# Kernel tuning notes

Measured on AMD Instinct MI355X. Metric: run time of the kernel, lower is better.

## Reference

```python
import jax, jax.numpy as jnp
import numpy as np

# Module hyperparameters (from init_kwargs)
KH = KW = 3
STRIDE = 2
PAD = 1
OUT_PAD = 1
DIL = 1
IN_LEN = 8   # length of each input capsule
OUT_LEN = 8  # length of each output capsule
N_IN_CAPS = 64 // IN_LEN    # 8
N_OUT_CAPS = 64 // OUT_LEN  # 8
NUM_ITERATIONS = 3


def _squash(x):
    # v * |v|^2 / ((1 + |v|^2) * |v|), along last (capsule-length) dim
    sn = jnp.sum(x * x, axis=-1, keepdims=True)
    return x * (sn / ((1.0 + sn) * jnp.sqrt(sn + 1e-12)))


def _k_means_routing(priors, num_iterations):
    # priors: [..., K, M] ; soft k-means routing with 'dot' similarity,
    # softmax over the votes dim K (softmax_dim=-2), squash at the end.
    out = jnp.mean(priors, axis=-2, keepdims=True)          # [..., 1, M]
    for _ in range(num_iterations):
        nrm = jnp.linalg.norm(out, axis=-1, keepdims=True)
        out_n = out / jnp.maximum(nrm, 1e-12)               # F.normalize(p=2)
        logits = jnp.sum(priors * out_n, axis=-1, keepdims=True)  # [..., K, 1]
        probs = jax.nn.softmax(logits, axis=-2)
        out = jnp.sum(probs * priors, axis=-2, keepdims=True)
    return _squash(out)[..., 0, :]                          # [..., M]


def setup_inputs() -> dict:
    key = jax.random.key(0)
    k1, k2, k3 = jax.random.split(key, 3)
    input = jax.random.normal(k1, (2, 64, 32, 32), dtype=jnp.float32)
    # weight: (in_length, out_channels//out_length, out_length, kh, kw)
    weight = jax.random.normal(k2, (IN_LEN, N_OUT_CAPS, OUT_LEN, KH, KW), dtype=jnp.float32) * 0.1
    # bias: (out_channels//out_length, out_length)
    bias = jax.random.normal(k3, (N_OUT_CAPS, OUT_LEN), dtype=jnp.float32) * 0.1
    return {"input": input, "weight": weight, "bias": bias}


def reference(input, weight, bias):
    n, c_in, h_in, w_in = input.shape
    fi = c_in // IN_LEN
    fo = weight.shape[1]
    # conv_transpose == conv(lhs-dilated input, spatially flipped kernel)
    pad_lo = DIL * (KH - 1) - PAD
    patches = jax.lax.conv_general_dilated_patches(
        input, (KH, KW), (1, 1),
        padding=((pad_lo, pad_lo + OUT_PAD), (pad_lo, pad_lo + OUT_PAD)),
        lhs_dilation=(STRIDE, STRIDE), rhs_dilation=(DIL, DIL))
    ho, wo = patches.shape[-2], patches.shape[-1]
    # feature dim of patches is ordered (c, kh, kw), channel-major
    patches = patches.reshape(n, fi, IN_LEN, KH, KW, ho, wo)
    w_flip = weight[..., ::-1, ::-1]  # [IN_LEN, fo, OUT_LEN, KH, KW]
    # votes: each (input capsule, kernel tap) casts a vote per output capsule
    priors = jnp.einsum('nflhwpq,lgmhw->npqgfhwm', patches, w_flip)
    priors = priors.reshape(n, ho, wo, fo, fi * KH * KW, OUT_LEN)
    out = _k_means_routing(priors, NUM_ITERATIONS)  # [n, ho, wo, fo, OUT_LEN]
    out = out + bias                                # bias: [fo, OUT_LEN]
    out = out.reshape(n, ho, wo, fo * OUT_LEN).transpose(0, 3, 1, 2)
    return out  # [n, out_channels, ho, wo] = [2, 64, 64, 64]
```

## Files before the change

### kernel.cpp

```cpp
#include <hip/hip_runtime.h>
#include <math.h>

#define HIN 32
#define WIN 32
#define NITER 3

#define IROW 96

typedef float f2 __attribute__((ext_vector_type(2)));
static __device__ __forceinline__ f2 mk2(float a, float b) { f2 r; r.x = a; r.y = b; return r; }
static __device__ __forceinline__ f2 fma2(f2 a, f2 b, f2 c) { return __builtin_elementwise_fma(a, b, c); }

template <int CTRL>
__device__ __forceinline__ float dpp_add(float v) {
    int p = __builtin_amdgcn_update_dpp(0, __float_as_int(v), CTRL, 0xF, 0xF, true);
    return v + __int_as_float(p);
}
__device__ __forceinline__ float sum8(float v) {
    v = dpp_add<0xB1>(v);
    v = dpp_add<0x4E>(v);
    v = dpp_add<0x141>(v);
    return v;
}

template <int TH, int TW>
__device__ __forceinline__ void stage_weights(const float* __restrict__ weight,
                                              float* __restrict__ wlds, int t) {
    constexpr int T = TH * TW;
    const int sg = (t >> 3) & 7;
    const int sm = t & 7;
    const int l0 = t >> 6;
    const int dbase = sg * 80 + (((sm >> 1) + (sg >> 1)) & 3) * 20 + (sm & 1);
#pragma unroll
    for (int k = 0; k < 2 * T; ++k) {
        const int vtap = k >> 1;
        const int chunk = k & 1;
        const int hh = (TH == 1) ? 1 : ((vtap / TW) * 2);
        const int ww = (TW == 1) ? 1 : ((vtap % TW) * 2);
        const int jflip = (2 - hh) * 3 + (2 - ww);
        const int l = chunk * 4 + l0;
        wlds[vtap * 640 + dbase + l * 2] = weight[(chunk * 256 + t) * 9 + jflip];
    }
}

template <int NROWS, int NCHUNK>
__device__ __forceinline__ void stage_input(const float* __restrict__ in,
                                            float* __restrict__ ilds,
                                            int t, int n, int y0, int x0) {
    const int c = t >> 2, r = t & 3;
    const int cpad = c + 4 * (c >> 3);
#pragma unroll
    for (int pp = r; pp < NROWS * NCHUNK; pp += 4) {
        const int yi = pp / NCHUNK, ch = pp % NCHUNK;
        const int y = y0 + yi;
        const int xc = x0 + ch * 4;
        float4 vv = {0.f, 0.f, 0.f, 0.f};
        if (y < HIN && xc < WIN)
            vv = *(const float4*)(in + (((size_t)(n * 64 + c) * HIN + y) * WIN + xc));
        ilds[(yi * 12 + ch * 4 + 0) * IROW + cpad] = vv.x;
        ilds[(yi * 12 + ch * 4 + 1) * IROW + cpad] = vv.y;
        ilds[(yi * 12 + ch * 4 + 2) * IROW + cpad] = vv.z;
        ilds[(yi * 12 + ch * 4 + 3) * IROW + cpad] = vv.w;
    }
}

template <int TH, int TW>
__device__ __forceinline__ void compute_pri(const float* __restrict__ ilds,
                                            const float* __restrict__ wlds,
                                            int q, int x0, int pi, int g, int s,
                                            f2 (&pri2)[TH * TW][4]) {
#pragma unroll
    for (int i = 0; i < TH; ++i) {
        const int y = (TH == 1) ? pi : (pi + i);
        const bool vy = (y < HIN);
#pragma unroll
        for (int j = 0; j < TW; ++j) {
            const int v = i * TW + j;
            const int w = (TW == 1) ? 1 : j * 2;
            const int x = (q + w - 1) >> 1;
            if (vy && x < WIN) {
                const float4* xp =
                    (const float4*)(ilds + (i * 12 + (x - x0)) * IROW + s * 12);
                float4 x0v = xp[0], x1v = xp[1];
                float xv[8] = {x0v.x, x0v.y, x0v.z, x0v.w, x1v.x, x1v.y, x1v.z, x1v.w};
                const float* wb = wlds + v * 640 + g * 80;
#pragma unroll
                for (int m2 = 0; m2 < 4; ++m2) {
                    const float4* row =
                        (const float4*)(wb + ((m2 + (g >> 1)) & 3) * 20);
                    f2 acc = mk2(0.f, 0.f);
#pragma unroll
                    for (int k = 0; k < 4; ++k) {
                        float4 w4 = row[k];
                        acc = fma2(mk2(xv[2 * k], xv[2 * k]), mk2(w4.x, w4.y), acc);
                        acc = fma2(mk2(xv[2 * k + 1], xv[2 * k + 1]), mk2(w4.z, w4.w), acc);
                    }
                    pri2[v][m2] = acc;
                }
            } else {
#pragma unroll
                for (int m2 = 0; m2 < 4; ++m2) pri2[v][m2] = mk2(0.f, 0.f);
            }
        }
    }
}

template <int T>
__device__ __forceinline__ float route_core(const f2 (&pri2)[T][4],
                                            const float* __restrict__ bias,
                                            int g, int s) {
    constexpr float Z = (float)(72 - 8 * T);
    f2 rr[4];
#pragma unroll
    for (int m2 = 0; m2 < 4; ++m2) {
        f2 a = mk2(0.f, 0.f);
#pragma unroll
        for (int v = 0; v < T; ++v) a += pri2[v][m2];
        rr[m2].x = sum8(a.x);
        rr[m2].y = sum8(a.y);
    }
    float r8v = 0.f;
#pragma unroll
    for (int it = 0; it < NITER; ++it) {
        f2 t2 = mk2(0.f, 0.f);
#pragma unroll
        for (int m2 = 0; m2 < 4; ++m2) t2 = fma2(rr[m2], rr[m2], t2);
        const float sn = t2.x + t2.y;
        const float inv = __builtin_amdgcn_rsqf(fmaxf(sn, 1e-24f)) * 1.44269504f;
        const f2 inv2 = mk2(inv, inv);
        f2 on2[4];
#pragma unroll
        for (int m2 = 0; m2 < 4; ++m2) on2[m2] = rr[m2] * inv2;

        float a8 = 0.f;
        f2 acc2[4];
#pragma unroll
        for (int m2 = 0; m2 < 4; ++m2) acc2[m2] = mk2(0.f, 0.f);
#pragma unroll
        for (int v = 0; v < T; ++v) {
            f2 d2 = mk2(0.f, 0.f);
#pragma unroll
            for (int m2 = 0; m2 < 4; ++m2) d2 = fma2(pri2[v][m2], on2[m2], d2);
            const float e = __builtin_exp2f(d2.x + d2.y);
            a8 += e;
            const f2 e2 = mk2(e, e);
#pragma unroll
            for (int m2 = 0; m2 < 4; ++m2) acc2[m2] = fma2(e2, pri2[v][m2], acc2[m2]);
        }
#pragma unroll
        for (int m2 = 0; m2 < 4; ++m2) {
            rr[m2].x = sum8(acc2[m2].x);
            rr[m2].y = sum8(acc2[m2].y);
        }
        if (it == NITER - 1) r8v = sum8(a8);
    }
    const float invs = __builtin_amdgcn_rcpf(r8v + Z);
    const f2 invs2 = mk2(invs, invs);
    f2 o2[4];
#pragma unroll
    for (int m2 = 0; m2 < 4; ++m2) o2[m2] = rr[m2] * invs2;
    f2 s2 = mk2(0.f, 0.f);
#pragma unroll
    for (int m2 = 0; m2 < 4; ++m2) s2 = fma2(o2[m2], o2[m2], s2);
    const float sn = s2.x + s2.y;
    const float factor =
        sn * __builtin_amdgcn_rcpf(1.f + sn) * __builtin_amdgcn_rsqf(sn + 1e-12f);
    f2 osel = o2[0];
#pragma unroll
    for (int m2 = 1; m2 < 4; ++m2)
        if ((s >> 1) == m2) osel = o2[m2];
    float val = (s & 1) ? osel.y : osel.x;
    return val * factor + bias[g * 8 + s];
}

template <int TH, int TW>
__device__ __forceinline__ void run_dual(
    const float* __restrict__ in, const float* __restrict__ weight,
    const float* __restrict__ bias, float* __restrict__ out,
    float* __restrict__ ilds, float* __restrict__ wlds, float* __restrict__ olds,
    int t, int n, int p, int pi, int qb, int x0) {
    constexpr int T = TH * TW;
    stage_input<TH, (TW == 2 ? 3 : 2)>(in, ilds, t, n, pi, x0);
    stage_weights<TH, TW>(weight, wlds, t);
    __syncthreads();

    const int wave = t >> 6;
    const int lane = t & 63;
    const int g = lane >> 3;
    const int s = lane & 7;
    const int qa = qb + 2 * wave;

    f2 pa[T][4], pb[T][4];
    compute_pri<TH, TW>(ilds, wlds, qa, x0, pi, g, s, pa);
    compute_pri<TH, TW>(ilds, wlds, qa + 8, x0, pi, g, s, pb);

    const float va = route_core<T>(pa, bias, g, s);
    const float vb = route_core<T>(pb, bias, g, s);

    olds[lane * 9 + wave] = va;
    olds[lane * 9 + wave + 4] = vb;
    __syncthreads();
    const int c2 = t >> 2, w = t & 3;
    float* ob = out + (((size_t)n * 64 + c2) * 64 + p) * 64 + qb;
    ob[2 * w] = olds[c2 * 9 + w];
    ob[2 * w + 8] = olds[c2 * 9 + w + 4];
}

__device__ __forceinline__ void run_t4(
    const float* __restrict__ in, const float* __restrict__ weight,
    const float* __restrict__ bias, float* __restrict__ out,
    float* __restrict__ ilds, float* __restrict__ wlds, float* __restrict__ olds,
    int t, int n, int p, int pi, int qb, int x0) {
    stage_input<2, 2>(in, ilds, t, n, pi, x0);
    stage_weights<2, 2>(weight, wlds, t);
    __syncthreads();

    const int wave = t >> 6;
    const int lane = t & 63;
    const int g = lane >> 3;
    const int s = lane & 7;

    f2 pa[4][4];
    compute_pri<2, 2>(ilds, wlds, qb + 2 * wave, x0, pi, g, s, pa);
    const float va = route_core<4>(pa, bias, g, s);

    olds[lane * 5 + wave] = va;
    __syncthreads();
    const int c2 = t >> 2, w = t & 3;
    out[(((size_t)n * 64 + c2) * 64 + p) * 64 + qb + 2 * w] = olds[c2 * 5 + w];
}

__global__ __launch_bounds__(256, 5) void caps_routing(
    const float* __restrict__ in, const float* __restrict__ weight,
    const float* __restrict__ bias, float* __restrict__ out) {
    __shared__ float ilds[2 * 12 * IROW];
    __shared__ float wlds[4 * 640];
    __shared__ float olds[576];
    const int t = threadIdx.x;

    const int b = blockIdx.x;
    const int grp = b / 5;
    const int sel = b - grp * 5;

    if (sel < 2) {
        const int idx = grp * 2 + sel;
        const int n = idx >> 8, r = idx & 255;
        const int pi = r >> 3, jq = r & 7;
        run_t4(in, weight, bias, out, ilds, wlds, olds,
               t, n, 2 * pi + 1, pi, 8 * jq + 1, 4 * jq);
    } else {
        const int n = grp >> 7, r = grp & 127;
        const int pi = r >> 2, jq = r & 3;
        if (sel == 2)
            run_dual<2, 1>(in, weight, bias, out, ilds, wlds, olds,
                           t, n, 2 * pi + 1, pi, 16 * jq, 8 * jq);
        else if (sel == 3)
            run_dual<1, 2>(in, weight, bias, out, ilds, wlds, olds,
                           t, n, 2 * pi, pi, 16 * jq + 1, 8 * jq);
        else
            run_dual<1, 1>(in, weight, bias, out, ilds, wlds, olds,
                           t, n, 2 * pi, pi, 16 * jq, 8 * jq);
    }
}

extern "C" void kernel_launch(void* const* d_in, const int* in_sizes, int n_in,
                              void* d_out, int out_size, void* d_ws, size_t ws_size,
                              hipStream_t stream) {
    const float* in = (const float*)d_in[0];
    const float* weight = (const float*)d_in[1];
    const float* bias = (const float*)d_in[2];
    float* out = (float*)d_out;
    (void)d_ws; (void)ws_size;

    caps_routing<<<1280, 256, 0, stream>>>(in, weight, bias, out);
}
```

Before: 66.48 us.

## Fuse dual-position prior computation to share weight loads and merge T4 path into dual

Computes priors for both output positions handled by a thread in one pass, so each weight row loaded from LDS is reused for two input vectors instead of being reloaded. The separate T=4 single-position path is removed and handled by a dual-position variant, cutting the grid from 1280 to 1024 blocks with a uniform four-way parity split. Launch bounds drop from 5 to 4 blocks per SIMD to allow more registers for the doubled prior arrays. Holding two 4-tap prior sets raises register pressure and lowers occupancy.

```diff
diff --git a/kernel.cpp b/kernel.cpp
--- a/kernel.cpp
+++ b/kernel.cpp
@@ -65,10 +65,11 @@
 }
 
 template <int TH, int TW>
-__device__ __forceinline__ void compute_pri(const float* __restrict__ ilds,
-                                            const float* __restrict__ wlds,
-                                            int q, int x0, int pi, int g, int s,
-                                            f2 (&pri2)[TH * TW][4]) {
+__device__ __forceinline__ void compute_pri_dual(const float* __restrict__ ilds,
+                                                 const float* __restrict__ wlds,
+                                                 int qa, int x0, int pi, int g, int s,
+                                                 f2 (&pa)[TH * TW][4],
+                                                 f2 (&pb)[TH * TW][4]) {
 #pragma unroll
     for (int i = 0; i < TH; ++i) {
         const int y = (TH == 1) ? pi : (pi + i);
@@ -77,29 +78,65 @@
         for (int j = 0; j < TW; ++j) {
             const int v = i * TW + j;
             const int w = (TW == 1) ? 1 : j * 2;
-            const int x = (q + w - 1) >> 1;
-            if (vy && x < WIN) {
+            const int xa = (qa + w - 1) >> 1;
+            const int xb = xa + 4;
+            const bool oka = vy && (xa < WIN);
+            const bool okb = vy && (xb < WIN);
+            float xva[8], xvb[8];
+            if (oka) {
                 const float4* xp =
-                    (const float4*)(ilds + (i * 12 + (x - x0)) * IROW + s * 12);
-                float4 x0v = xp[0], x1v = xp[1];
-                float xv[8] = {x0v.x, x0v.y, x0v.z, x0v.w, x1v.x, x1v.y, x1v.z, x1v.w};
+                    (const float4*)(ilds + (i * 12 + (xa - x0)) * IROW + s * 12);
+                float4 u0 = xp[0], u1 = xp[1];
+                xva[0] = u0.x; xva[1] = u0.y; xva[2] = u0.z; xva[3] = u0.w;
+                xva[4] = u1.x; xva[5] = u1.y; xva[6] = u1.z; xva[7] = u1.w;
+            }
+            if (okb) {
+                const float4* xp =
+                    (const float4*)(ilds + (i * 12 + (xb - x0)) * IROW + s * 12);
+                float4 u0 = xp[0], u1 = xp[1];
+                xvb[0] = u0.x; xvb[1] = u0.y; xvb[2] = u0.z; xvb[3] = u0.w;
+                xvb[4] = u1.x; xvb[5] = u1.y; xvb[6] = u1.z; xvb[7] = u1.w;
+            }
+            if (oka || okb) {
                 const float* wb = wlds + v * 640 + g * 80;
 #pragma unroll
                 for (int m2 = 0; m2 < 4; ++m2) {
                     const float4* row =
                         (const float4*)(wb + ((m2 + (g >> 1)) & 3) * 20);
-                    f2 acc = mk2(0.f, 0.f);
-#pragma unroll
-                    for (int k = 0; k < 4; ++k) {
-                        float4 w4 = row[k];
-                        acc = fma2(mk2(xv[2 * k], xv[2 * k]), mk2(w4.x, w4.y), acc);
-                        acc = fma2(mk2(xv[2 * k + 1], xv[2 * k + 1]), mk2(w4.z, w4.w), acc);
+                    float4 rw[4] = {row[0], row[1], row[2], row[3]};
+                    if (oka) {
+                        f2 acc = mk2(0.f, 0.f);
+#pragma unroll
+                        for (int k = 0; k < 4; ++k) {
+                            acc = fma2(mk2(xva[2 * k], xva[2 * k]),
+                                       mk2(rw[k].x, rw[k].y), acc);
+                            acc = fma2(mk2(xva[2 * k + 1], xva[2 * k + 1]),
+                                       mk2(rw[k].z, rw[k].w), acc);
+                        }
+                        pa[v][m2] = acc;
+                    } else {
+                        pa[v][m2] = mk2(0.f, 0.f);
                     }
-                    pri2[v][m2] = acc;
+                    if (okb) {
+                        f2 acc = mk2(0.f, 0.f);
+#pragma unroll
+                        for (int k = 0; k < 4; ++k) {
+                            acc = fma2(mk2(xvb[2 * k], xvb[2 * k]),
+                                       mk2(rw[k].x, rw[k].y), acc);
+                            acc = fma2(mk2(xvb[2 * k + 1], xvb[2 * k + 1]),
+                                       mk2(rw[k].z, rw[k].w), acc);
+                        }
+                        pb[v][m2] = acc;
+                    } else {
+                        pb[v][m2] = mk2(0.f, 0.f);
+                    }
                 }
             } else {
 #pragma unroll
-                for (int m2 = 0; m2 < 4; ++m2) pri2[v][m2] = mk2(0.f, 0.f);
+                for (int m2 = 0; m2 < 4; ++m2) {
+                    pa[v][m2] = mk2(0.f, 0.f);
+                    pb[v][m2] = mk2(0.f, 0.f);
+                }
             }
         }
     }
@@ -191,8 +228,7 @@
     const int qa = qb + 2 * wave;
 
     f2 pa[T][4], pb[T][4];
-    compute_pri<TH, TW>(ilds, wlds, qa, x0, pi, g, s, pa);
-    compute_pri<TH, TW>(ilds, wlds, qa + 8, x0, pi, g, s, pb);
+    compute_pri_dual<TH, TW>(ilds, wlds, qa, x0, pi, g, s, pa, pb);
 
     const float va = route_core<T>(pa, bias, g, s);
     const float vb = route_core<T>(pb, bias, g, s);
@@ -206,31 +242,7 @@
     ob[2 * w + 8] = olds[c2 * 9 + w + 4];
 }
 
-__device__ __forceinline__ void run_t4(
-    const float* __restrict__ in, const float* __restrict__ weight,
-    const float* __restrict__ bias, float* __restrict__ out,
-    float* __restrict__ ilds, float* __restrict__ wlds, float* __restrict__ olds,
-    int t, int n, int p, int pi, int qb, int x0) {
-    stage_input<2, 2>(in, ilds, t, n, pi, x0);
-    stage_weights<2, 2>(weight, wlds, t);
-    __syncthreads();
-
-    const int wave = t >> 6;
-    const int lane = t & 63;
-    const int g = lane >> 3;
-    const int s = lane & 7;
-
-    f2 pa[4][4];
-    compute_pri<2, 2>(ilds, wlds, qb + 2 * wave, x0, pi, g, s, pa);
-    const float va = route_core<4>(pa, bias, g, s);
-
-    olds[lane * 5 + wave] = va;
-    __syncthreads();
-    const int c2 = t >> 2, w = t & 3;
-    out[(((size_t)n * 64 + c2) * 64 + p) * 64 + qb + 2 * w] = olds[c2 * 5 + w];
-}
-
-__global__ __launch_bounds__(256, 5) void caps_routing(
+__global__ __launch_bounds__(256, 4) void caps_routing(
     const float* __restrict__ in, const float* __restrict__ weight,
     const float* __restrict__ bias, float* __restrict__ out) {
     __shared__ float ilds[2 * 12 * IROW];
@@ -239,28 +251,25 @@
     const int t = threadIdx.x;
 
     const int b = blockIdx.x;
-    const int grp = b / 5;
-    const int sel = b - grp * 5;
-
-    if (sel < 2) {
-        const int idx = grp * 2 + sel;
-        const int n = idx >> 8, r = idx & 255;
-        const int pi = r >> 3, jq = r & 7;
-        run_t4(in, weight, bias, out, ilds, wlds, olds,
-               t, n, 2 * pi + 1, pi, 8 * jq + 1, 4 * jq);
-    } else {
-        const int n = grp >> 7, r = grp & 127;
-        const int pi = r >> 2, jq = r & 3;
-        if (sel == 2)
-            run_dual<2, 1>(in, weight, bias, out, ilds, wlds, olds,
-                           t, n, 2 * pi + 1, pi, 16 * jq, 8 * jq);
-        else if (sel == 3)
-            run_dual<1, 2>(in, weight, bias, out, ilds, wlds, olds,
-                           t, n, 2 * pi, pi, 16 * jq + 1, 8 * jq);
-        else
-            run_dual<1, 1>(in, weight, bias, out, ilds, wlds, olds,
-                           t, n, 2 * pi, pi, 16 * jq, 8 * jq);
-    }
+    const int sel = b & 3;
+    const int grp = b >> 2;
+    const int n = grp >> 7;
+    const int r = grp & 127;
+    const int pi = r >> 2;
+    const int jq = r & 3;
+
+    if (sel == 0)
+        run_dual<2, 2>(in, weight, bias, out, ilds, wlds, olds,
+                       t, n, 2 * pi + 1, pi, 16 * jq + 1, 8 * jq);
+    else if (sel == 1)
+        run_dual<2, 1>(in, weight, bias, out, ilds, wlds, olds,
+                       t, n, 2 * pi + 1, pi, 16 * jq, 8 * jq);
+    else if (sel == 2)
+        run_dual<1, 2>(in, weight, bias, out, ilds, wlds, olds,
+                       t, n, 2 * pi, pi, 16 * jq + 1, 8 * jq);
+    else
+        run_dual<1, 1>(in, weight, bias, out, ilds, wlds, olds,
+                       t, n, 2 * pi, pi, 16 * jq, 8 * jq);
 }
 
 extern "C" void kernel_launch(void* const* d_in, const int* in_sizes, int n_in,
@@ -272,5 +281,5 @@
     float* out = (float*)d_out;
     (void)d_ws; (void)ws_size;
 
-    caps_routing<<<1280, 256, 0, stream>>>(in, weight, bias, out);
-}
+    caps_routing<<<1024, 256, 0, stream>>>(in, weight, bias, out);
+}
```

New measurement: 69.57 us. +4.6%, slower.
